# Optimization experiments

Hardware: AMD Instinct MI355X
Metric: run time of the kernel (lower is better)

## Reference

```python
import jax, jax.numpy as jnp
import numpy as np

EPS = 1e-8


def setup_inputs() -> dict:
    key = jax.random.key(0)
    k1, k2 = jax.random.split(key)
    x = jax.random.normal(k1, (32, 16, 4096), dtype=jnp.float32)
    # shapelets param: (in_channels, num_shapelets, shapelets_size)
    shapelets = jax.random.normal(k2, (16, 64, 64), dtype=jnp.float32)
    return {"x": x, "shapelets": shapelets}


def reference(x, shapelets):
    # x: (B, C, L); shapelets: (C, K, S)
    S = shapelets.shape[2]
    C = x.shape[1]
    W = x.shape[2] - S + 1
    # sliding windows, equivalent to torch unfold(2, S, 1): (B, C, W, S)
    idx = jnp.arange(W)[:, None] + jnp.arange(S)[None, :]
    win = x[:, :, idx]
    win = win / jnp.maximum(jnp.linalg.norm(win, axis=3, keepdims=True), EPS)
    sh = shapelets / jnp.maximum(jnp.linalg.norm(shapelets, axis=2, keepdims=True), EPS)
    # pairwise cosine dot, then mean over channels: (B, W, K)
    sim = jnp.einsum('bcws,cks->bwk', win, sh) / C
    # relu then global max over window positions; torch keeps the summed dim -> (B, 1, K)
    out = jnp.max(jax.nn.relu(sim), axis=1)[:, None, :]
    return out
```

## Files before the change

### kernel.cpp

```cpp
#include <hip/hip_runtime.h>

typedef unsigned int u32;
typedef unsigned short u16;
typedef __bf16 bf16x8 __attribute__((ext_vector_type(8)));
typedef float f32x4 __attribute__((ext_vector_type(4)));

static __device__ __forceinline__ u16 f2bf(float f) {
  u32 u = __float_as_uint(f);
  return (u16)((u + 0x7fffu + ((u >> 16) & 1u)) >> 16);
}
static __device__ __forceinline__ float b2f(u16 v) {
  return __uint_as_float(((u32)v) << 16);
}
static __device__ __forceinline__ u32 pk2(u16 lo, u16 hi) {
  return (u32)lo | ((u32)hi << 16);
}

__global__ __launch_bounds__(256) void prep_kernel(const float* __restrict__ sh,
                                                   u16* __restrict__ shn2,
                                                   float* __restrict__ out) {
  if (blockIdx.x == 0) {
    float4 z = {0.f, 0.f, 0.f, 0.f};
    *(float4*)&out[threadIdx.x * 8] = z;
    *(float4*)&out[threadIdx.x * 8 + 4] = z;
  }
  const int s = threadIdx.x & 63;
  const int wv = threadIdx.x >> 6;
  const int row0 = blockIdx.x * 16 + wv * 4;
#pragma unroll
  for (int r = 0; r < 4; ++r) {
    const int row = row0 + r;
    float v = sh[row * 64 + s];
    float ss = v * v;
#pragma unroll
    for (int o = 1; o < 64; o <<= 1) ss += __shfl_xor(ss, o, 64);
    float iw = 1.0f / fmaxf(sqrtf(ss), 1e-8f);
    const int c = row >> 6, k = row & 63;
    const int chunk = c * 8 + (k >> 4) * 2 + (s >> 5);
    const int pos = ((k & 15) + (((s & 31) >> 3) << 4)) * 8 + (s & 7);
    shn2[chunk * 512 + pos] = f2bf(v * iw);
  }
}

#define WT 256
#define CSTRIDE 168
#define SSTRIDE 2728

__global__ __launch_bounds__(512, 3) void main_kernel(const float* __restrict__ x,
                                                      const u16* __restrict__ shn2,
                                                      float* __restrict__ out) {
  __shared__ u32 xs[4 * SSTRIDE];
  __shared__ u16 invwb[16 * WT];
  __shared__ int redbuf[64];

  const int tid = threadIdx.x;
  const int lane = tid & 63;
  const int wid = tid >> 6;
  const int w0 = blockIdx.x * WT;
  const int b = blockIdx.y;
  const float* xb = x + (size_t)b * 16 * 4096;

  if (tid < 64) redbuf[tid] = 0;

  {
    const int q = tid & 31;
    const int c = tid >> 5;
    if (q < 20) {
      const float* xc = xb + c * 4096;
      const int e0 = w0 + 16 * q;
      float xv[20];
      if (e0 + 19 < 4096) {
#pragma unroll
        for (int r = 0; r < 5; ++r) *(float4*)&xv[4 * r] = *(const float4*)&xc[e0 + 4 * r];
      } else {
#pragma unroll
        for (int j = 0; j < 20; ++j) {
          int g = e0 + j;
          xv[j] = xc[g < 4096 ? g : 4095];
        }
      }
      u16 bf[20];
#pragma unroll
      for (int j = 0; j < 20; ++j) bf[j] = f2bf(xv[j]);
#pragma unroll
      for (int s = 0; s < 4; ++s) {
        u32 pk[8];
#pragma unroll
        for (int r = 0; r < 8; ++r) pk[r] = pk2(bf[2 * r + s], bf[2 * r + s + 1]);
        u32* dst = &xs[s * SSTRIDE + c * CSTRIDE + 8 * q];
        *(uint4*)dst = make_uint4(pk[0], pk[1], pk[2], pk[3]);
        *(uint4*)(dst + 4) = make_uint4(pk[4], pk[5], pk[6], pk[7]);
      }
    }
  }

  {
    const int c = tid >> 5;
    const int wb = (tid & 31) * 8;
    const float* xc = xb + c * 4096;
    const int e0 = w0 + wb;
    float hd[8], tl[8], ss = 0.f;
    if (e0 + 71 < 4096) {
#pragma unroll
      for (int r = 0; r < 16; ++r) {
        float4 v = *(const float4*)&xc[e0 + 4 * r];
        if (r < 2) {
          hd[4 * r + 0] = v.x; hd[4 * r + 1] = v.y;
          hd[4 * r + 2] = v.z; hd[4 * r + 3] = v.w;
        }
        ss += v.x * v.x + v.y * v.y + v.z * v.z + v.w * v.w;
      }
#pragma unroll
      for (int r = 0; r < 2; ++r) {
        float4 v = *(const float4*)&xc[e0 + 64 + 4 * r];
        tl[4 * r + 0] = v.x; tl[4 * r + 1] = v.y;
        tl[4 * r + 2] = v.z; tl[4 * r + 3] = v.w;
      }
    } else {
#pragma unroll
      for (int j = 0; j < 72; ++j) {
        int g = e0 + j;
        float v = xc[g < 4096 ? g : 4095];
        if (j < 8) hd[j] = v;
        if (j >= 64) tl[j - 64] = v;
        if (j < 64) ss += v * v;
      }
    }
    u16 ov[8];
#pragma unroll
    for (int i = 0; i < 8; ++i) {
      float iw = 0.0625f / fmaxf(sqrtf(fmaxf(ss, 0.f)), 1e-8f);
      ov[i] = (e0 + i < 4033) ? f2bf(iw) : (u16)0;
      ss += tl[i] * tl[i] - hd[i] * hd[i];
    }
    *(uint4*)&invwb[c * WT + wb] = make_uint4(pk2(ov[0], ov[1]), pk2(ov[2], ov[3]),
                                              pk2(ov[4], ov[5]), pk2(ov[6], ov[7]));
  }

  __syncthreads();

  f32x4 acc[4][2];
#pragma unroll
  for (int mt = 0; mt < 4; ++mt)
#pragma unroll
    for (int nt = 0; nt < 2; ++nt) acc[mt][nt] = (f32x4){0.f, 0.f, 0.f, 0.f};

  const int m = lane & 15;
  const int h = lane >> 4;
  const int wgrp = wid >> 1;
  const int kgrp = wid & 1;
  const u32* xbase = xs + (m & 3) * SSTRIDE;
  const int joff = 32 * wgrp + 2 * (m >> 2) + 4 * h;
  const u16* shb = shn2 + lane * 8 + kgrp * 2 * 1024;
  const int iwbase = 64 * wgrp + 4 * h;

  for (int c = 0; c < 16; ++c) {
    const u32* xc = xbase + c * CSTRIDE;
    bf16x8 af[6];
#pragma unroll
    for (int f = 0; f < 6; ++f) {
      const u32* p = xc + joff + 8 * f;
      uint2 lo = *(const uint2*)p;
      uint2 hi = *(const uint2*)(p + 2);
      af[f] = __builtin_bit_cast(bf16x8, make_uint4(lo.x, lo.y, hi.x, hi.y));
    }
    f32x4 iwq[4];
#pragma unroll
    for (int mt = 0; mt < 4; ++mt) {
      ushort4 r4 = *(const ushort4*)&invwb[c * WT + iwbase + 16 * mt];
      iwq[mt] = (f32x4){b2f(r4.x), b2f(r4.y), b2f(r4.z), b2f(r4.w)};
    }
    const u16* sc = shb + c * 4096;
#pragma unroll
    for (int nt = 0; nt < 2; ++nt) {
      bf16x8 b0 = __builtin_bit_cast(bf16x8, *(const uint4*)(sc + (nt * 2 + 0) * 512));
      bf16x8 b1 = __builtin_bit_cast(bf16x8, *(const uint4*)(sc + (nt * 2 + 1) * 512));
#pragma unroll
      for (int mt = 0; mt < 4; ++mt) {
        f32x4 d = {0.f, 0.f, 0.f, 0.f};
        d = __builtin_amdgcn_mfma_f32_16x16x32_bf16(af[mt],     b0, d, 0, 0, 0);
        d = __builtin_amdgcn_mfma_f32_16x16x32_bf16(af[mt + 2], b1, d, 0, 0, 0);
        acc[mt][nt] += iwq[mt] * d;
      }
    }
  }

#pragma unroll
  for (int nt = 0; nt < 2; ++nt) {
    float v = 0.f;
#pragma unroll
    for (int mt = 0; mt < 4; ++mt)
      v = fmaxf(v, fmaxf(fmaxf(acc[mt][nt].x, acc[mt][nt].y),
                         fmaxf(acc[mt][nt].z, acc[mt][nt].w)));
    v = fmaxf(v, __shfl_xor(v, 16, 64));
    v = fmaxf(v, __shfl_xor(v, 32, 64));
    if (lane < 16) atomicMax(&redbuf[kgrp * 32 + nt * 16 + lane], __float_as_int(v));
  }
  __syncthreads();
  if (tid < 64) atomicMax((int*)&out[b * 64 + tid], redbuf[tid]);
}

extern "C" void kernel_launch(void* const* d_in, const int* in_sizes, int n_in,
                              void* d_out, int out_size, void* d_ws, size_t ws_size,
                              hipStream_t stream) {
  const float* x = (const float*)d_in[0];
  const float* sh = (const float*)d_in[1];
  float* out = (float*)d_out;
  u16* shn2 = (u16*)d_ws;

  prep_kernel<<<dim3(64), dim3(256), 0, stream>>>(sh, shn2, out);
  main_kernel<<<dim3(16, 32), dim3(512), 0, stream>>>(x, shn2, out);
}
```

Baseline: 41.33 us.

## Split channel loop across wave pairs and reduce partial sums via LDS

Waves previously split the 64 shapelets into two halves and each looped over all 16 channels. Now each wave pair splits the channels instead, so each wave does 8 channels for all 64 shapelets. The two halves of the partial sums are then added through an LDS staging buffer in four synchronised rounds before the relu/max reduction. The per-window inverse norms are also stored as fp32 instead of bf16, which removes the unpack and improves precision. In exchange the kernel doubles its accumulator registers and adds 64 KB of LDS, which drops the occupancy target from 3 to 2 blocks per CU, and it adds extra barriers.

```diff
diff --git a/kernel.cpp b/kernel.cpp
--- a/kernel.cpp
+++ b/kernel.cpp
@@ -8,9 +8,6 @@
 static __device__ __forceinline__ u16 f2bf(float f) {
   u32 u = __float_as_uint(f);
   return (u16)((u + 0x7fffu + ((u >> 16) & 1u)) >> 16);
-}
-static __device__ __forceinline__ float b2f(u16 v) {
-  return __uint_as_float(((u32)v) << 16);
 }
 static __device__ __forceinline__ u32 pk2(u16 lo, u16 hi) {
   return (u32)lo | ((u32)hi << 16);
@@ -45,12 +42,14 @@
 #define WT 256
 #define CSTRIDE 168
 #define SSTRIDE 2728
-
-__global__ __launch_bounds__(512, 3) void main_kernel(const float* __restrict__ x,
+#define IWS 264
+
+__global__ __launch_bounds__(512, 2) void main_kernel(const float* __restrict__ x,
                                                       const u16* __restrict__ shn2,
                                                       float* __restrict__ out) {
   __shared__ u32 xs[4 * SSTRIDE];
-  __shared__ u16 invwb[16 * WT];
+  __shared__ float invwb[16 * IWS];
+  __shared__ float red2[4][4][64][4];
   __shared__ int redbuf[64];
 
   const int tid = threadIdx.x;
@@ -126,35 +125,36 @@
         if (j < 64) ss += v * v;
       }
     }
-    u16 ov[8];
+    float ov[8];
 #pragma unroll
     for (int i = 0; i < 8; ++i) {
       float iw = 0.0625f / fmaxf(sqrtf(fmaxf(ss, 0.f)), 1e-8f);
-      ov[i] = (e0 + i < 4033) ? f2bf(iw) : (u16)0;
+      ov[i] = (e0 + i < 4033) ? iw : 0.f;
       ss += tl[i] * tl[i] - hd[i] * hd[i];
     }
-    *(uint4*)&invwb[c * WT + wb] = make_uint4(pk2(ov[0], ov[1]), pk2(ov[2], ov[3]),
-                                              pk2(ov[4], ov[5]), pk2(ov[6], ov[7]));
+    *(float4*)&invwb[c * IWS + wb] = make_float4(ov[0], ov[1], ov[2], ov[3]);
+    *(float4*)&invwb[c * IWS + wb + 4] = make_float4(ov[4], ov[5], ov[6], ov[7]);
   }
 
   __syncthreads();
 
-  f32x4 acc[4][2];
+  f32x4 acc[4][4];
 #pragma unroll
   for (int mt = 0; mt < 4; ++mt)
 #pragma unroll
-    for (int nt = 0; nt < 2; ++nt) acc[mt][nt] = (f32x4){0.f, 0.f, 0.f, 0.f};
+    for (int nt = 0; nt < 4; ++nt) acc[mt][nt] = (f32x4){0.f, 0.f, 0.f, 0.f};
 
   const int m = lane & 15;
   const int h = lane >> 4;
   const int wgrp = wid >> 1;
-  const int kgrp = wid & 1;
+  const int cgrp = wid & 1;
   const u32* xbase = xs + (m & 3) * SSTRIDE;
   const int joff = 32 * wgrp + 2 * (m >> 2) + 4 * h;
-  const u16* shb = shn2 + lane * 8 + kgrp * 2 * 1024;
+  const u16* shb = shn2 + lane * 8;
   const int iwbase = 64 * wgrp + 4 * h;
 
-  for (int c = 0; c < 16; ++c) {
+  for (int i = 0; i < 8; ++i) {
+    const int c = cgrp * 8 + i;
     const u32* xc = xbase + c * CSTRIDE;
     bf16x8 af[6];
 #pragma unroll
@@ -166,13 +166,11 @@
     }
     f32x4 iwq[4];
 #pragma unroll
-    for (int mt = 0; mt < 4; ++mt) {
-      ushort4 r4 = *(const ushort4*)&invwb[c * WT + iwbase + 16 * mt];
-      iwq[mt] = (f32x4){b2f(r4.x), b2f(r4.y), b2f(r4.z), b2f(r4.w)};
-    }
+    for (int mt = 0; mt < 4; ++mt)
+      iwq[mt] = *(const f32x4*)&invwb[c * IWS + iwbase + 16 * mt];
     const u16* sc = shb + c * 4096;
 #pragma unroll
-    for (int nt = 0; nt < 2; ++nt) {
+    for (int nt = 0; nt < 4; ++nt) {
       bf16x8 b0 = __builtin_bit_cast(bf16x8, *(const uint4*)(sc + (nt * 2 + 0) * 512));
       bf16x8 b1 = __builtin_bit_cast(bf16x8, *(const uint4*)(sc + (nt * 2 + 1) * 512));
 #pragma unroll
@@ -186,15 +184,33 @@
   }
 
 #pragma unroll
-  for (int nt = 0; nt < 2; ++nt) {
-    float v = 0.f;
-#pragma unroll
-    for (int mt = 0; mt < 4; ++mt)
-      v = fmaxf(v, fmaxf(fmaxf(acc[mt][nt].x, acc[mt][nt].y),
-                         fmaxf(acc[mt][nt].z, acc[mt][nt].w)));
-    v = fmaxf(v, __shfl_xor(v, 16, 64));
-    v = fmaxf(v, __shfl_xor(v, 32, 64));
-    if (lane < 16) atomicMax(&redbuf[kgrp * 32 + nt * 16 + lane], __float_as_int(v));
+  for (int mt = 0; mt < 4; ++mt) {
+    if (cgrp) {
+#pragma unroll
+      for (int nt = 0; nt < 4; ++nt)
+        *(f32x4*)&red2[wgrp][nt][lane][0] = acc[mt][nt];
+    }
+    __syncthreads();
+    if (!cgrp) {
+#pragma unroll
+      for (int nt = 0; nt < 4; ++nt)
+        acc[mt][nt] += *(const f32x4*)&red2[wgrp][nt][lane][0];
+    }
+    __syncthreads();
+  }
+
+  if (!cgrp) {
+#pragma unroll
+    for (int nt = 0; nt < 4; ++nt) {
+      float v = 0.f;
+#pragma unroll
+      for (int mt = 0; mt < 4; ++mt)
+        v = fmaxf(v, fmaxf(fmaxf(acc[mt][nt].x, acc[mt][nt].y),
+                           fmaxf(acc[mt][nt].z, acc[mt][nt].w)));
+      v = fmaxf(v, __shfl_xor(v, 16, 64));
+      v = fmaxf(v, __shfl_xor(v, 32, 64));
+      if (lane < 16) atomicMax(&redbuf[nt * 16 + lane], __float_as_int(v));
+    }
   }
   __syncthreads();
   if (tid < 64) atomicMax((int*)&out[b * 64 + tid], redbuf[tid]);
```

New measurement: 114.9 us. 178% more time.
